# Kernel optimization log

Measured on AMD Instinct MI355X. Metric: run time of the kernel, lower is better.

## Reference

```python
import jax, jax.numpy as jnp
import numpy as np
import math

D_MODEL = 1024
N_HEADS = 16
D_K = D_MODEL // N_HEADS
B, S = 2, 2048


def setup_inputs() -> dict:
    key = jax.random.key(0)
    ks = jax.random.split(key, 11)
    sc = 1.0 / math.sqrt(D_MODEL)
    inp = {
        'q': jax.random.normal(ks[0], (B, S, D_MODEL), jnp.float32),
        'k': jax.random.normal(ks[1], (B, S, D_MODEL), jnp.float32),
        'v': jax.random.normal(ks[2], (B, S, D_MODEL), jnp.float32),
        'mask': jnp.tril(jnp.ones((S, S), jnp.int32))[None, None],  # [1,1,S,S] causal
        'W_q': jax.random.normal(ks[3], (D_MODEL, D_MODEL), jnp.float32) * sc,
        'b_q': jnp.zeros((D_MODEL,), jnp.float32),
        'W_k': jax.random.normal(ks[4], (D_MODEL, D_MODEL), jnp.float32) * sc,
        'b_k': jnp.zeros((D_MODEL,), jnp.float32),
        'W_v': jax.random.normal(ks[5], (D_MODEL, D_MODEL), jnp.float32) * sc,
        'b_v': jnp.zeros((D_MODEL,), jnp.float32),
        'W_o': jax.random.normal(ks[6], (D_MODEL, D_MODEL), jnp.float32) * sc,
        'b_o': jnp.zeros((D_MODEL,), jnp.float32),
    }
    return inp


def reference(q, k, v, mask, W_q, b_q, W_k, b_k, W_v, b_v, W_o, b_o):
    # Linear projections then split heads: [B,S,D] -> [B,H,S,d_k]
    def split_heads(x):
        b, s, _ = x.shape
        return x.reshape(b, s, N_HEADS, D_K).transpose(0, 2, 1, 3)

    Q = split_heads(q @ W_q + b_q)
    K = split_heads(k @ W_k + b_k)
    V = split_heads(v @ W_v + b_v)

    scores = jnp.einsum('bhqd,bhkd->bhqk', Q, K) / math.sqrt(D_K)
    scores = jnp.where(mask == 0, jnp.float32(-1e9), scores)
    attn = jax.nn.softmax(scores, axis=-1)  # dropout is identity in eval mode
    out = jnp.einsum('bhqk,bhkd->bhqd', attn, V)
    out = out.transpose(0, 2, 1, 3).reshape(q.shape[0], -1, D_MODEL)
    return out @ W_o + b_o
```

## Files before the change

kernel.cpp:

```cpp
#include <hip/hip_runtime.h>
#include <hip/hip_bf16.h>

#define D_MODEL 1024
#define S_LEN   2048
#define BATCH   2
#define NH      16
#define DK      64

typedef __bf16 bf16_t;
typedef __attribute__((ext_vector_type(8))) __bf16 bf16x8;
typedef __attribute__((ext_vector_type(4))) float f32x4;

#if __has_builtin(__builtin_amdgcn_exp2f)
#define EXP2F(x) __builtin_amdgcn_exp2f(x)
#else
#define EXP2F(x) exp2f(x)
#endif

#define Q_SCALE 0.1803368801111204f

#define GLDS16(gp, lp) __builtin_amdgcn_global_load_lds( \
    (const __attribute__((address_space(1))) void*)(gp), \
    (__attribute__((address_space(3))) void*)(lp), 16, 0, 0)

__global__ __launch_bounds__(256) void cvt_qkv(const float* __restrict__ q,
                                               const float* __restrict__ k,
                                               const float* __restrict__ v,
                                               bf16_t* __restrict__ out) {
    const long NELEM = (long)BATCH * S_LEN * D_MODEL;
    const float* src = (blockIdx.y == 0) ? q : (blockIdx.y == 1) ? k : v;
    long i = ((long)blockIdx.x * 256 + threadIdx.x) * 8;
    float4 a = *(const float4*)(src + i);
    float4 b = *(const float4*)(src + i + 4);
    bf16x8 o;
    o[0] = (bf16_t)a.x; o[1] = (bf16_t)a.y; o[2] = (bf16_t)a.z; o[3] = (bf16_t)a.w;
    o[4] = (bf16_t)b.x; o[5] = (bf16_t)b.y; o[6] = (bf16_t)b.z; o[7] = (bf16_t)b.w;
    *(bf16x8*)(out + blockIdx.y * NELEM + i) = o;
}

__global__ void wt_transpose4(const float* __restrict__ Wq, const float* __restrict__ Wk,
                              const float* __restrict__ Wv, const float* __restrict__ Wo,
                              bf16_t* __restrict__ WqkvT, bf16_t* __restrict__ WoT) {
    __shared__ float t[32][33];
    const float* in = (blockIdx.z == 0) ? Wq : (blockIdx.z == 1) ? Wk
                    : (blockIdx.z == 2) ? Wv : Wo;
    bf16_t* out = (blockIdx.z < 3) ? (WqkvT + (long)blockIdx.z * D_MODEL * D_MODEL) : WoT;
    int tx = threadIdx.x, ty = threadIdx.y;
    int gx = blockIdx.x * 32, gy = blockIdx.y * 32;
#pragma unroll
    for (int i = 0; i < 32; i += 8)
        t[ty + i][tx] = in[(gy + ty + i) * D_MODEL + gx + tx];
    __syncthreads();
#pragma unroll
    for (int i = 0; i < 32; i += 8)
        out[(gx + ty + i) * D_MODEL + gy + tx] = (bf16_t)t[tx][ty + i];
}

__global__ void v_transpose(const bf16_t* __restrict__ in, bf16_t* __restrict__ out) {
    __shared__ bf16_t t[32][33];
    int tx = threadIdx.x, ty = threadIdx.y;
    int bh = blockIdx.z;
    int s0 = blockIdx.x * 32, d0 = blockIdx.y * 32;
    const bf16_t* ip = in + (long)bh * S_LEN * DK;
    bf16_t* op = out + (long)bh * DK * S_LEN;
#pragma unroll
    for (int i = 0; i < 32; i += 8)
        t[ty + i][tx] = ip[(long)(s0 + ty + i) * DK + d0 + tx];
    __syncthreads();
#pragma unroll
    for (int i = 0; i < 32; i += 8)
        op[(long)(d0 + ty + i) * S_LEN + s0 + tx] = t[tx][ty + i];
}

#define BM 128
#define BN 128
#define BKT 64

__device__ __forceinline__ void swizzle_xy(int bx, int by, int& n0, int& m0) {
    int lin = by * 8 + bx;
    n0 = (lin >> 5) * BN;
    m0 = (lin & 31) * BM;
}

__device__ __forceinline__ void stage_swz(const bf16_t* __restrict__ G, int row0,
                                          int k0, bf16_t* __restrict__ Ls, int tid) {
#pragma unroll
    for (int it = 0; it < 4; ++it) {
        int g = it * 256 + tid;
        int row = g >> 3;
        int c = (g & 7) ^ (row & 7);
        GLDS16(&G[(long)(row0 + row) * D_MODEL + k0 + c * 8],
               &Ls[(it * 256 + (tid & ~63)) * 8]);
    }
}

__device__ __forceinline__ bf16x8 frag_swz(const bf16_t* __restrict__ Ls, int row, int cg) {
    return *(const bf16x8*)(&Ls[(row * 8 + (cg ^ (row & 7))) * 8]);
}

__global__ __launch_bounds__(256) void gemm_qkv(
    const bf16_t* __restrict__ qkvb, const bf16_t* __restrict__ WqkvT,
    const float* __restrict__ bq, const float* __restrict__ bk, const float* __restrict__ bv,
    bf16_t* __restrict__ Qw, bf16_t* __restrict__ Kw, bf16_t* __restrict__ Vw)
{
    __shared__ __align__(16) bf16_t As[BM * BKT];
    __shared__ __align__(16) bf16_t Bs[BN * BKT];
    const int z = blockIdx.z;
    const bf16_t* A  = qkvb + (long)z * BATCH * S_LEN * D_MODEL;
    const bf16_t* BT = WqkvT + (long)z * D_MODEL * D_MODEL;
    const float* bias = (z == 0) ? bq : (z == 1) ? bk : bv;
    bf16_t* Cb = (z == 0) ? Qw : (z == 1) ? Kw : Vw;
    const float oscale = (z == 0) ? Q_SCALE : 1.0f;

    const int tid  = threadIdx.x;
    const int wave = tid >> 6, lane = tid & 63;
    const int lrow = lane & 15, kgrp = lane >> 4;
    const int wm = (wave >> 1) * 64, wn = (wave & 1) * 64;
    int m0, n0;
    swizzle_xy(blockIdx.x, blockIdx.y, n0, m0);

    f32x4 acc[4][4] = {};

    for (int k0 = 0; k0 < D_MODEL; k0 += BKT) {
        stage_swz(A, m0, k0, As, tid);
        stage_swz(BT, n0, k0, Bs, tid);
        __syncthreads();
#pragma unroll
        for (int kk = 0; kk < 2; ++kk) {
            bf16x8 af[4], bfr[4];
#pragma unroll
            for (int mi = 0; mi < 4; ++mi)
                af[mi] = frag_swz(As, wm + mi * 16 + lrow, kk * 4 + kgrp);
#pragma unroll
            for (int ni = 0; ni < 4; ++ni)
                bfr[ni] = frag_swz(Bs, wn + ni * 16 + lrow, kk * 4 + kgrp);
#pragma unroll
            for (int mi = 0; mi < 4; ++mi)
#pragma unroll
                for (int ni = 0; ni < 4; ++ni)
                    acc[mi][ni] = __builtin_amdgcn_mfma_f32_16x16x32_bf16(af[mi], bfr[ni], acc[mi][ni], 0, 0, 0);
        }
        __syncthreads();
    }

#pragma unroll
    for (int mi = 0; mi < 4; ++mi)
#pragma unroll
        for (int ni = 0; ni < 4; ++ni) {
            int col = n0 + wn + ni * 16 + lrow;
            float bvf = bias[col];
#pragma unroll
            for (int r = 0; r < 4; ++r) {
                int row = m0 + wm + mi * 16 + kgrp * 4 + r;
                float vv = (acc[mi][ni][r] + bvf) * oscale;
                int b = row >> 11, s = row & (S_LEN - 1);
                int h = col >> 6, d = col & (DK - 1);
                Cb[(((long)(b * NH + h) * S_LEN + s) * DK) + d] = (bf16_t)vv;
            }
        }
}

__global__ __launch_bounds__(256) void gemm_out(
    const bf16_t* __restrict__ A, const bf16_t* __restrict__ BT,
    const float* __restrict__ bias, float* __restrict__ Cf)
{
    __shared__ __align__(16) bf16_t As[BM * BKT];
    __shared__ __align__(16) bf16_t Bs[BN * BKT];
    const int tid  = threadIdx.x;
    const int wave = tid >> 6, lane = tid & 63;
    const int lrow = lane & 15, kgrp = lane >> 4;
    const int wm = (wave >> 1) * 64, wn = (wave & 1) * 64;
    int m0, n0;
    swizzle_xy(blockIdx.x, blockIdx.y, n0, m0);

    f32x4 acc[4][4] = {};

    for (int k0 = 0; k0 < D_MODEL; k0 += BKT) {
        stage_swz(A, m0, k0, As, tid);
        stage_swz(BT, n0, k0, Bs, tid);
        __syncthreads();
#pragma unroll
        for (int kk = 0; kk < 2; ++kk) {
            bf16x8 af[4], bfr[4];
#pragma unroll
            for (int mi = 0; mi < 4; ++mi)
                af[mi] = frag_swz(As, wm + mi * 16 + lrow, kk * 4 + kgrp);
#pragma unroll
            for (int ni = 0; ni < 4; ++ni)
                bfr[ni] = frag_swz(Bs, wn + ni * 16 + lrow, kk * 4 + kgrp);
#pragma unroll
            for (int mi = 0; mi < 4; ++mi)
#pragma unroll
                for (int ni = 0; ni < 4; ++ni)
                    acc[mi][ni] = __builtin_amdgcn_mfma_f32_16x16x32_bf16(af[mi], bfr[ni], acc[mi][ni], 0, 0, 0);
        }
        __syncthreads();
    }

#pragma unroll
    for (int mi = 0; mi < 4; ++mi)
#pragma unroll
        for (int ni = 0; ni < 4; ++ni) {
            int col = n0 + wn + ni * 16 + lrow;
            float bvf = bias[col];
#pragma unroll
            for (int r = 0; r < 4; ++r) {
                int row = m0 + wm + mi * 16 + kgrp * 4 + r;
                Cf[(long)row * D_MODEL + col] = acc[mi][ni][r] + bvf;
            }
        }
}

__device__ __forceinline__ void attn_one_qtile(
    int qi, int bh, int wave, int lrow, int kgrp,
    int r0, int c0, int r1,
    const bf16_t* __restrict__ Qh, const bf16_t* __restrict__ Kh,
    const bf16_t* __restrict__ Vth, bf16_t* __restrict__ O,
    bf16_t* __restrict__ Ks, bf16_t* __restrict__ Vs, bf16_t* __restrict__ Pw)
{
    const int q0 = qi * 64;
    const int qrow = q0 + wave * 16;

    bf16x8 qf[2];
#pragma unroll
    for (int kk = 0; kk < 2; ++kk)
        qf[kk] = *(const bf16x8*)(&Qh[(qrow + lrow) * DK + kk * 32 + kgrp * 8]);

    f32x4 acc[4] = {};
    float lsum[4] = {0.f, 0.f, 0.f, 0.f};

    const int nt = qi + 1;

    uint4 kpre0 = *(const uint4*)(&Kh[(long)r0 * DK + c0]);
    uint4 kpre1 = *(const uint4*)(&Kh[(long)r1 * DK + c0]);
    uint4 vpre0 = *(const uint4*)(&Vth[(long)r0 * S_LEN + c0]);
    uint4 vpre1 = *(const uint4*)(&Vth[(long)r1 * S_LEN + c0]);

    for (int t = 0; t < nt; ++t) {
        __syncthreads();
        *(uint4*)(&Ks[r0 * 72 + c0]) = kpre0;
        *(uint4*)(&Ks[r1 * 72 + c0]) = kpre1;
        *(uint4*)(&Vs[r0 * 72 + c0]) = vpre0;
        *(uint4*)(&Vs[r1 * 72 + c0]) = vpre1;
        if (t + 1 < nt) {
            const int j0n = (t + 1) * 64;
            kpre0 = *(const uint4*)(&Kh[(long)(j0n + r0) * DK + c0]);
            kpre1 = *(const uint4*)(&Kh[(long)(j0n + r1) * DK + c0]);
            vpre0 = *(const uint4*)(&Vth[(long)r0 * S_LEN + j0n + c0]);
            vpre1 = *(const uint4*)(&Vth[(long)r1 * S_LEN + j0n + c0]);
        }
        __syncthreads();

        const int j0 = t * 64;

        f32x4 sc[4] = {};
#pragma unroll
        for (int kk = 0; kk < 2; ++kk)
#pragma unroll
            for (int ni = 0; ni < 4; ++ni) {
                bf16x8 kf = *(const bf16x8*)(&Ks[(ni * 16 + lrow) * 72 + kk * 32 + kgrp * 8]);
                sc[ni] = __builtin_amdgcn_mfma_f32_16x16x32_bf16(qf[kk], kf, sc[ni], 0, 0, 0);
            }

        const bool needmask = (j0 + 63 > qrow);
        if (needmask) {
#pragma unroll
            for (int r = 0; r < 4; ++r) {
                int row = qrow + kgrp * 4 + r;
#pragma unroll
                for (int ni = 0; ni < 4; ++ni) {
                    int colj = j0 + ni * 16 + lrow;
                    float pv = EXP2F(sc[ni][r]);
                    if (colj > row) pv = 0.f;
                    lsum[r] += pv;
                    Pw[(kgrp * 4 + r) * 72 + ni * 16 + lrow] = (bf16_t)pv;
                }
            }
        } else {
#pragma unroll
            for (int r = 0; r < 4; ++r)
#pragma unroll
                for (int ni = 0; ni < 4; ++ni) {
                    float pv = EXP2F(sc[ni][r]);
                    lsum[r] += pv;
                    Pw[(kgrp * 4 + r) * 72 + ni * 16 + lrow] = (bf16_t)pv;
                }
        }

#pragma unroll
        for (int kk = 0; kk < 2; ++kk) {
            bf16x8 pf = *(const bf16x8*)(&Pw[lrow * 72 + kk * 32 + kgrp * 8]);
#pragma unroll
            for (int di = 0; di < 4; ++di) {
                bf16x8 vf = *(const bf16x8*)(&Vs[(di * 16 + lrow) * 72 + kk * 32 + kgrp * 8]);
                acc[di] = __builtin_amdgcn_mfma_f32_16x16x32_bf16(pf, vf, acc[di], 0, 0, 0);
            }
        }
    }

#pragma unroll
    for (int r = 0; r < 4; ++r)
#pragma unroll
        for (int off = 1; off < 16; off <<= 1)
            lsum[r] += __shfl_xor(lsum[r], off);

    const int b = bh >> 4, h = bh & (NH - 1);
#pragma unroll
    for (int r = 0; r < 4; ++r) {
        int s = qrow + kgrp * 4 + r;
        float inv = 1.f / lsum[r];
#pragma unroll
        for (int di = 0; di < 4; ++di) {
            int d = di * 16 + lrow;
            O[((long)(b * S_LEN + s)) * D_MODEL + h * DK + d] = (bf16_t)(acc[di][r] * inv);
        }
    }
}

__global__ __launch_bounds__(256, 2) void attn_kernel(
    const bf16_t* __restrict__ Q, const bf16_t* __restrict__ K,
    const bf16_t* __restrict__ Vt, bf16_t* __restrict__ O)
{
    __shared__ __align__(16) bf16_t Ks[64 * 72];
    __shared__ __align__(16) bf16_t Vs[64 * 72];
    __shared__ __align__(16) bf16_t Ps[4][16 * 72];

    const int bh = blockIdx.y;
    const int p  = blockIdx.x;
    const int tid = threadIdx.x, wave = tid >> 6, lane = tid & 63;
    const int lrow = lane & 15, kgrp = lane >> 4;

    const bf16_t* Qh  = Q  + (long)bh * S_LEN * DK;
    const bf16_t* Kh  = K  + (long)bh * S_LEN * DK;
    const bf16_t* Vth = Vt + (long)bh * DK * S_LEN;

    const int f0 = tid * 8;
    const int r0 = f0 >> 6, c0 = f0 & 63;
    const int r1 = (f0 + 2048) >> 6;

    attn_one_qtile(31 - p, bh, wave, lrow, kgrp, r0, c0, r1,
                   Qh, Kh, Vth, O, Ks, Vs, Ps[wave]);
    attn_one_qtile(p, bh, wave, lrow, kgrp, r0, c0, r1,
                   Qh, Kh, Vth, O, Ks, Vs, Ps[wave]);
}

extern "C" void kernel_launch(void* const* d_in, const int* in_sizes, int n_in,
                              void* d_out, int out_size, void* d_ws, size_t ws_size,
                              hipStream_t stream) {
    const float* q  = (const float*)d_in[0];
    const float* k  = (const float*)d_in[1];
    const float* v  = (const float*)d_in[2];
    const float* Wq = (const float*)d_in[4];
    const float* bq = (const float*)d_in[5];
    const float* Wk = (const float*)d_in[6];
    const float* bk = (const float*)d_in[7];
    const float* Wv = (const float*)d_in[8];
    const float* bv = (const float*)d_in[9];
    const float* Wo = (const float*)d_in[10];
    const float* bo = (const float*)d_in[11];

    char* ws = (char*)d_ws;
    const size_t Mi = 1024 * 1024;
    bf16_t* WqkvT = (bf16_t*)(ws);
    bf16_t* WoT   = (bf16_t*)(ws + 6 * Mi);
    bf16_t* Qw    = (bf16_t*)(ws + 8 * Mi);
    bf16_t* Kw    = (bf16_t*)(ws + 16 * Mi);
    bf16_t* Vw    = (bf16_t*)(ws + 24 * Mi);
    bf16_t* qkvb  = (bf16_t*)(ws + 32 * Mi);
    bf16_t* Vtw   = (bf16_t*)(ws + 32 * Mi);
    bf16_t* Aw    = (bf16_t*)(ws + 24 * Mi);

    const long NELEM = (long)BATCH * S_LEN * D_MODEL;
    cvt_qkv<<<dim3((int)(NELEM / 2048), 3), 256, 0, stream>>>(q, k, v, qkvb);

    dim3 tb(32, 8);
    wt_transpose4<<<dim3(D_MODEL / 32, D_MODEL / 32, 4), tb, 0, stream>>>(
        Wq, Wk, Wv, Wo, WqkvT, WoT);

    gemm_qkv<<<dim3(D_MODEL / BN, (BATCH * S_LEN) / BM, 3), 256, 0, stream>>>(
        qkvb, WqkvT, bq, bk, bv, Qw, Kw, Vw);

    v_transpose<<<dim3(S_LEN / 32, DK / 32, BATCH * NH), tb, 0, stream>>>(Vw, Vtw);

    attn_kernel<<<dim3(16, BATCH * NH), 256, 0, stream>>>(Qw, Kw, Vtw, Aw);

    gemm_out<<<dim3(D_MODEL / BN, (BATCH * S_LEN) / BM), 256, 0, stream>>>(
        Aw, WoT, bo, (float*)d_out);
}
```

Before: 239.2 us.

## Split attention into one q-tile per block, shrink output GEMM tile, add MFMA priority

The attention kernel now launches one block per 64-row query tile instead of pairing a long and a short tile per block. It raises the occupancy hint to 4 blocks per SIMD group and issues blocks longest-first to balance the causal work. The output projection GEMM uses 64-row M tiles, doubling its block count to fill more compute units. s_setprio is raised around the MFMA sections so waves doing matrix math get issue priority. The risks are imbalance from uneven causal tiles, register pressure under the tighter launch bound, and less data reuse per block in the smaller GEMM tile.

```diff
diff --git a/kernel.cpp b/kernel.cpp
--- a/kernel.cpp
+++ b/kernel.cpp
@@ -82,10 +82,11 @@
     m0 = (lin & 31) * BM;
 }
 
+template <int ROWS>
 __device__ __forceinline__ void stage_swz(const bf16_t* __restrict__ G, int row0,
                                           int k0, bf16_t* __restrict__ Ls, int tid) {
 #pragma unroll
-    for (int it = 0; it < 4; ++it) {
+    for (int it = 0; it < ROWS / 32; ++it) {
         int g = it * 256 + tid;
         int row = g >> 3;
         int c = (g & 7) ^ (row & 7);
@@ -122,8 +123,8 @@
     f32x4 acc[4][4] = {};
 
     for (int k0 = 0; k0 < D_MODEL; k0 += BKT) {
-        stage_swz(A, m0, k0, As, tid);
-        stage_swz(BT, n0, k0, Bs, tid);
+        stage_swz<BM>(A, m0, k0, As, tid);
+        stage_swz<BN>(BT, n0, k0, Bs, tid);
         __syncthreads();
 #pragma unroll
         for (int kk = 0; kk < 2; ++kk) {
@@ -160,36 +161,38 @@
         }
 }
 
+#define OM 64
 __global__ __launch_bounds__(256) void gemm_out(
     const bf16_t* __restrict__ A, const bf16_t* __restrict__ BT,
     const float* __restrict__ bias, float* __restrict__ Cf)
 {
-    __shared__ __align__(16) bf16_t As[BM * BKT];
+    __shared__ __align__(16) bf16_t As[OM * BKT];
     __shared__ __align__(16) bf16_t Bs[BN * BKT];
     const int tid  = threadIdx.x;
     const int wave = tid >> 6, lane = tid & 63;
     const int lrow = lane & 15, kgrp = lane >> 4;
-    const int wm = (wave >> 1) * 64, wn = (wave & 1) * 64;
-    int m0, n0;
-    swizzle_xy(blockIdx.x, blockIdx.y, n0, m0);
-
-    f32x4 acc[4][4] = {};
+    const int wm = (wave >> 1) * 32, wn = (wave & 1) * 64;
+    int lin = blockIdx.y * 8 + blockIdx.x;
+    int m0 = (lin & 63) * OM;
+    int n0 = (lin >> 6) * BN;
+
+    f32x4 acc[2][4] = {};
 
     for (int k0 = 0; k0 < D_MODEL; k0 += BKT) {
-        stage_swz(A, m0, k0, As, tid);
-        stage_swz(BT, n0, k0, Bs, tid);
+        stage_swz<OM>(A, m0, k0, As, tid);
+        stage_swz<BN>(BT, n0, k0, Bs, tid);
         __syncthreads();
 #pragma unroll
         for (int kk = 0; kk < 2; ++kk) {
-            bf16x8 af[4], bfr[4];
-#pragma unroll
-            for (int mi = 0; mi < 4; ++mi)
+            bf16x8 af[2], bfr[4];
+#pragma unroll
+            for (int mi = 0; mi < 2; ++mi)
                 af[mi] = frag_swz(As, wm + mi * 16 + lrow, kk * 4 + kgrp);
 #pragma unroll
             for (int ni = 0; ni < 4; ++ni)
                 bfr[ni] = frag_swz(Bs, wn + ni * 16 + lrow, kk * 4 + kgrp);
 #pragma unroll
-            for (int mi = 0; mi < 4; ++mi)
+            for (int mi = 0; mi < 2; ++mi)
 #pragma unroll
                 for (int ni = 0; ni < 4; ++ni)
                     acc[mi][ni] = __builtin_amdgcn_mfma_f32_16x16x32_bf16(af[mi], bfr[ni], acc[mi][ni], 0, 0, 0);
@@ -198,7 +201,7 @@
     }
 
 #pragma unroll
-    for (int mi = 0; mi < 4; ++mi)
+    for (int mi = 0; mi < 2; ++mi)
 #pragma unroll
         for (int ni = 0; ni < 4; ++ni) {
             int col = n0 + wn + ni * 16 + lrow;
@@ -254,6 +257,7 @@
         const int j0 = t * 64;
 
         f32x4 sc[4] = {};
+        __builtin_amdgcn_s_setprio(1);
 #pragma unroll
         for (int kk = 0; kk < 2; ++kk)
 #pragma unroll
@@ -261,6 +265,7 @@
                 bf16x8 kf = *(const bf16x8*)(&Ks[(ni * 16 + lrow) * 72 + kk * 32 + kgrp * 8]);
                 sc[ni] = __builtin_amdgcn_mfma_f32_16x16x32_bf16(qf[kk], kf, sc[ni], 0, 0, 0);
             }
+        __builtin_amdgcn_s_setprio(0);
 
         const bool needmask = (j0 + 63 > qrow);
         if (needmask) {
@@ -287,6 +292,7 @@
                 }
         }
 
+        __builtin_amdgcn_s_setprio(1);
 #pragma unroll
         for (int kk = 0; kk < 2; ++kk) {
             bf16x8 pf = *(const bf16x8*)(&Pw[lrow * 72 + kk * 32 + kgrp * 8]);
@@ -296,6 +302,7 @@
                 acc[di] = __builtin_amdgcn_mfma_f32_16x16x32_bf16(pf, vf, acc[di], 0, 0, 0);
             }
         }
+        __builtin_amdgcn_s_setprio(0);
     }
 
 #pragma unroll
@@ -317,7 +324,7 @@
     }
 }
 
-__global__ __launch_bounds__(256, 2) void attn_kernel(
+__global__ __launch_bounds__(256, 4) void attn_kernel(
     const bf16_t* __restrict__ Q, const bf16_t* __restrict__ K,
     const bf16_t* __restrict__ Vt, bf16_t* __restrict__ O)
 {
@@ -326,7 +333,7 @@
     __shared__ __align__(16) bf16_t Ps[4][16 * 72];
 
     const int bh = blockIdx.y;
-    const int p  = blockIdx.x;
+    const int qi = 31 - blockIdx.x;
     const int tid = threadIdx.x, wave = tid >> 6, lane = tid & 63;
     const int lrow = lane & 15, kgrp = lane >> 4;
 
@@ -338,9 +345,7 @@
     const int r0 = f0 >> 6, c0 = f0 & 63;
     const int r1 = (f0 + 2048) >> 6;
 
-    attn_one_qtile(31 - p, bh, wave, lrow, kgrp, r0, c0, r1,
-                   Qh, Kh, Vth, O, Ks, Vs, Ps[wave]);
-    attn_one_qtile(p, bh, wave, lrow, kgrp, r0, c0, r1,
+    attn_one_qtile(qi, bh, wave, lrow, kgrp, r0, c0, r1,
                    Qh, Kh, Vth, O, Ks, Vs, Ps[wave]);
 }
 
@@ -382,8 +387,8 @@
 
     v_transpose<<<dim3(S_LEN / 32, DK / 32, BATCH * NH), tb, 0, stream>>>(Vw, Vtw);
 
-    attn_kernel<<<dim3(16, BATCH * NH), 256, 0, stream>>>(Qw, Kw, Vtw, Aw);
-
-    gemm_out<<<dim3(D_MODEL / BN, (BATCH * S_LEN) / BM), 256, 0, stream>>>(
+    attn_kernel<<<dim3(32, BATCH * NH), 256, 0, stream>>>(Qw, Kw, Vtw, Aw);
+
+    gemm_out<<<dim3(D_MODEL / BN, (BATCH * S_LEN) / OM), 256, 0, stream>>>(
         Aw, WoT, bo, (float*)d_out);
 }
```

Result: slower. 257.5 us (+7.6%).
